# Performance work log

Hardware: AMD Instinct MI355X
Metric: run time of the kernel (lower is better)

Reference implementation:

```python
import jax, jax.numpy as jnp
import numpy as np

N = 20000   # mesh vertices
B = 8       # batch
F = 64      # in_channels
K = 6       # Chebyshev order
OUT = 64    # out_channels
NNZ = 320000  # nonzeros in sparse Laplacian (avg degree 16)


def setup_inputs() -> dict:
    key = jax.random.key(0)
    ks = jax.random.split(key, 6)
    x = jax.random.normal(ks[0], (B, N, F), dtype=jnp.float32)
    lap_rows = jax.random.randint(ks[1], (NNZ,), 0, N, dtype=jnp.int32)
    lap_cols = jax.random.randint(ks[2], (NNZ,), 0, N, dtype=jnp.int32)
    lap_vals = jax.random.normal(ks[3], (NNZ,), dtype=jnp.float32) * 0.05
    # fc: Linear(K*F, OUT), xavier_normal weight, zero bias
    W = jax.random.normal(ks[4], (OUT, K * F), dtype=jnp.float32) * float(np.sqrt(2.0 / (K * F + OUT)))
    b = jnp.zeros((OUT,), dtype=jnp.float32)
    return {"x": x, "lap_rows": lap_rows, "lap_cols": lap_cols,
            "lap_vals": lap_vals, "W": W, "b": b}


def reference(x, lap_rows, lap_cols, lap_vals, W, b):
    Bd, Nd, Fd = x.shape

    def spmm(v):  # sparse [N,N] @ dense [N, B*F] via COO gather + segment_sum
        return jax.ops.segment_sum(lap_vals[:, None] * v[lap_cols], lap_rows,
                                   num_segments=Nd)

    x0 = jnp.transpose(x, (1, 0, 2)).reshape(Nd, Bd * Fd)  # [N, B*F]
    outs = [x0]
    if K > 1:
        tx1 = spmm(x0)
        outs.append(tx1)
        tx0 = x0
        for _ in range(2, K):  # Chebyshev recurrence T_k = 2 L T_{k-1} - T_{k-2}
            tx2 = 2.0 * spmm(tx1) - tx0
            outs.append(tx2)
            tx0, tx1 = tx1, tx2
    out = jnp.concatenate([o.reshape(Nd, Bd, Fd) for o in outs], axis=2)  # [N,B,K*F]
    out = out.reshape(Nd * Bd, K * Fd) @ W.T + b  # dense fc
    return jnp.transpose(out.reshape(Nd, Bd, -1), (1, 0, 2))  # [B,N,OUT]
```

## Files before the change

kernel.cpp:

```cpp
#include <hip/hip_runtime.h>

#define N_V  20000
#define B_   8
#define F_   64
#define K_   6
#define OUT_ 64
#define NNZ_ 320000
#define BF   512
#define NSLICE 8
#define SLICE_W 2500
#define NBUK (N_V * NSLICE)
#define SCANB 157

typedef unsigned short ushort_t;
typedef unsigned int   uint_t;

using frag_ab = __attribute__((ext_vector_type(8))) short;
using frag_cd = __attribute__((ext_vector_type(4))) float;

__device__ __forceinline__ ushort_t f2bf(float f) {
    uint_t u = __float_as_uint(f);
    u += 0x7FFFu + ((u >> 16) & 1u);
    return (ushort_t)(u >> 16);
}
__device__ __forceinline__ uint_t pack2(float lo, float hi) {
    return (uint_t)f2bf(lo) | ((uint_t)f2bf(hi) << 16);
}
__device__ __forceinline__ void unpack2(uint_t u, float& lo, float& hi) {
    lo = __uint_as_float(u << 16);
    hi = __uint_as_float(u & 0xFFFF0000u);
}


__global__ void hist_kernel(const int* __restrict__ rows, const int* __restrict__ cols,
                            int* __restrict__ counts) {
    int e = blockIdx.x * 256 + threadIdx.x;
    if (e < NNZ_) {
        int key = (cols[e] / SLICE_W) * N_V + rows[e];
        atomicAdd(&counts[key], 1);
    }
}

__global__ __launch_bounds__(1024) void scan1(const int* __restrict__ counts,
                                              int* __restrict__ incl, int* __restrict__ bsum) {
    __shared__ int buf[1024];
    int tid = threadIdx.x;
    int i = blockIdx.x * 1024 + tid;
    int c = (i < NBUK) ? counts[i] : 0;
    buf[tid] = c;
    __syncthreads();
    for (int off = 1; off < 1024; off <<= 1) {
        int t = buf[tid];
        int add = (tid >= off) ? buf[tid - off] : 0;
        __syncthreads();
        buf[tid] = t + add;
        __syncthreads();
    }
    if (i < NBUK) incl[i] = buf[tid];
    if (tid == 1023) bsum[blockIdx.x] = buf[1023];
}

__global__ __launch_bounds__(256) void scan2(int* __restrict__ bsum) {
    __shared__ int buf[256];
    int tid = threadIdx.x;
    int c = (tid < SCANB) ? bsum[tid] : 0;
    buf[tid] = c;
    __syncthreads();
    for (int off = 1; off < 256; off <<= 1) {
        int t = buf[tid];
        int add = (tid >= off) ? buf[tid - off] : 0;
        __syncthreads();
        buf[tid] = t + add;
        __syncthreads();
    }
    if (tid < SCANB) bsum[tid] = buf[tid] - c;
}

__global__ __launch_bounds__(1024) void scan3(const int* __restrict__ counts,
                                              const int* __restrict__ bsum,
                                              int* __restrict__ bp, int* __restrict__ cursor) {
    int tid = threadIdx.x;
    int i = blockIdx.x * 1024 + tid;
    if (i < NBUK) {
        int p = bsum[blockIdx.x] + cursor[i];
        bp[i + 1] = p;
        cursor[i] = p - counts[i];
    }
    if (i == 0) bp[0] = 0;
}

__global__ void scatter_kernel(const int* __restrict__ rows, const int* __restrict__ cols,
                               const float* __restrict__ vals, int* __restrict__ cursor,
                               int2* __restrict__ edges) {
    int e = blockIdx.x * 256 + threadIdx.x;
    if (e < NNZ_) {
        int c = cols[e];
        int key = (c / SLICE_W) * N_V + rows[e];
        int pos = atomicAdd(&cursor[key], 1);
        int2 pe;
        pe.x = c;
        pe.y = __float_as_int(vals[e]);
        edges[pos] = pe;
    }
}

__global__ void prep_kernel(const float* __restrict__ x, uint_t* __restrict__ X0,
                            const float* __restrict__ W, ushort_t* __restrict__ Wfrag) {
    int blk = blockIdx.x;
    if (blk < 20000) {
        int idx = blk * 256 + threadIdx.x;
        int f2 = idx & 31;
        int b  = (idx >> 5) & 7;
        int n  = idx >> 8;
        float2 v = *(const float2*)&x[((size_t)b * N_V + n) * F_ + f2 * 2];
        X0[n * 256 + b * 32 + f2] = pack2(v.x, v.y);
    } else {
        int idx = (blk - 20000) * 256 + threadIdx.x;
        if (idx < 12 * 4 * 64 * 8) {
            int j    = idx & 7;
            int lane = (idx >> 3) & 63;
            int ct   = (idx >> 9) & 3;
            int s    = idx >> 11;
            int o     = ct * 16 + (lane & 15);
            int kglob = s * 32 + ((lane >> 4) & 3) * 8 + j;
            Wfrag[idx] = f2bf(W[o * (K_ * F_) + kglob]);
        }
    }
}

template <bool RECUR>
__global__ __launch_bounds__(256) void cheb_phase(const int* __restrict__ bp,
                                                  const int2* __restrict__ edges,
                                                  const ushort_t* __restrict__ Tprev,
                                                  const ushort_t* __restrict__ Tpp,
                                                  ushort_t* __restrict__ Tout) {
    const int wave = threadIdx.x >> 6, lane = threadIdx.x & 63;
    const int n0 = blockIdx.x * 8 + wave * 2;
    const int fo = lane * 8;

    float a0[8], a1[8];
#pragma unroll
    for (int i = 0; i < 8; ++i) { a0[i] = 0.f; a1[i] = 0.f; }

    for (int s = 0; s < NSLICE; ++s) {
        const int base = s * N_V + n0;
        const int st  = bp[base];
        const int mid = bp[base + 1];
        const int en  = bp[base + 2];
        for (int j = st; j < en; j += 4) {
            const int j1 = j + 1, j2 = j + 2, j3 = j + 3;
            const int c1 = min(j1, en - 1), c2 = min(j2, en - 1), c3 = min(j3, en - 1);
            int2 E0 = edges[j];
            int2 E1 = edges[c1];
            int2 E2 = edges[c2];
            int2 E3 = edges[c3];
            float v0 = __int_as_float(E0.y);
            float v1 = (j1 < en) ? __int_as_float(E1.y) : 0.f;
            float v2 = (j2 < en) ? __int_as_float(E2.y) : 0.f;
            float v3 = (j3 < en) ? __int_as_float(E3.y) : 0.f;
            uint4 u0 = *(const uint4*)(Tprev + (size_t)E0.x * BF + fo);
            uint4 u1 = *(const uint4*)(Tprev + (size_t)E1.x * BF + fo);
            uint4 u2 = *(const uint4*)(Tprev + (size_t)E2.x * BF + fo);
            uint4 u3 = *(const uint4*)(Tprev + (size_t)E3.x * BF + fo);
            float p00 = (j  < mid) ? v0 : 0.f, p01 = (j  < mid) ? 0.f : v0;
            float p10 = (j1 < mid) ? v1 : 0.f, p11 = (j1 < mid) ? 0.f : v1;
            float p20 = (j2 < mid) ? v2 : 0.f, p21 = (j2 < mid) ? 0.f : v2;
            float p30 = (j3 < mid) ? v3 : 0.f, p31 = (j3 < mid) ? 0.f : v3;
            float e0[8], e1[8], e2[8], e3[8];
            unpack2(u0.x, e0[0], e0[1]); unpack2(u0.y, e0[2], e0[3]);
            unpack2(u0.z, e0[4], e0[5]); unpack2(u0.w, e0[6], e0[7]);
            unpack2(u1.x, e1[0], e1[1]); unpack2(u1.y, e1[2], e1[3]);
            unpack2(u1.z, e1[4], e1[5]); unpack2(u1.w, e1[6], e1[7]);
            unpack2(u2.x, e2[0], e2[1]); unpack2(u2.y, e2[2], e2[3]);
            unpack2(u2.z, e2[4], e2[5]); unpack2(u2.w, e2[6], e2[7]);
            unpack2(u3.x, e3[0], e3[1]); unpack2(u3.y, e3[2], e3[3]);
            unpack2(u3.z, e3[4], e3[5]); unpack2(u3.w, e3[6], e3[7]);
#pragma unroll
            for (int i = 0; i < 8; ++i) {
                a0[i] = fmaf(p00, e0[i], a0[i]);
                a1[i] = fmaf(p01, e0[i], a1[i]);
                a0[i] = fmaf(p10, e1[i], a0[i]);
                a1[i] = fmaf(p11, e1[i], a1[i]);
                a0[i] = fmaf(p20, e2[i], a0[i]);
                a1[i] = fmaf(p21, e2[i], a1[i]);
                a0[i] = fmaf(p30, e3[i], a0[i]);
                a1[i] = fmaf(p31, e3[i], a1[i]);
            }
        }
    }

    {
        float res[8];
#pragma unroll
        for (int i = 0; i < 8; ++i) res[i] = a0[i];
        if (RECUR) {
            uint4 up = *(const uint4*)(Tpp + (size_t)n0 * BF + fo);
            float ep[8];
            unpack2(up.x, ep[0], ep[1]); unpack2(up.y, ep[2], ep[3]);
            unpack2(up.z, ep[4], ep[5]); unpack2(up.w, ep[6], ep[7]);
#pragma unroll
            for (int i = 0; i < 8; ++i) res[i] = 2.f * res[i] - ep[i];
        }
        uint4 st4;
        st4.x = pack2(res[0], res[1]);
        st4.y = pack2(res[2], res[3]);
        st4.z = pack2(res[4], res[5]);
        st4.w = pack2(res[6], res[7]);
        *(uint4*)(Tout + (size_t)n0 * BF + fo) = st4;
    }
    {
        float res[8];
#pragma unroll
        for (int i = 0; i < 8; ++i) res[i] = a1[i];
        if (RECUR) {
            uint4 up = *(const uint4*)(Tpp + (size_t)(n0 + 1) * BF + fo);
            float ep[8];
            unpack2(up.x, ep[0], ep[1]); unpack2(up.y, ep[2], ep[3]);
            unpack2(up.z, ep[4], ep[5]); unpack2(up.w, ep[6], ep[7]);
#pragma unroll
            for (int i = 0; i < 8; ++i) res[i] = 2.f * res[i] - ep[i];
        }
        uint4 st4;
        st4.x = pack2(res[0], res[1]);
        st4.y = pack2(res[2], res[3]);
        st4.z = pack2(res[4], res[5]);
        st4.w = pack2(res[6], res[7]);
        *(uint4*)(Tout + (size_t)(n0 + 1) * BF + fo) = st4;
    }
}

__global__ __launch_bounds__(256) void fc_mfma(const ushort_t* __restrict__ X0,
                                               const ushort_t* __restrict__ T1,
                                               const ushort_t* __restrict__ T2,
                                               const ushort_t* __restrict__ T3,
                                               const ushort_t* __restrict__ T4,
                                               const ushort_t* __restrict__ T5,
                                               const ushort_t* __restrict__ Wfrag,
                                               const float* __restrict__ bias,
                                               float* __restrict__ out) {
    const int wave = threadIdx.x >> 6, lane = threadIdx.x & 63;
    const int quad = lane >> 4, col = lane & 15;
    const int tb = blockIdx.x * 128 + wave * 32;
    const int r0 = tb + col, r1 = tb + 16 + col;
    const ushort_t* Tbuf[6] = {X0, T1, T2, T3, T4, T5};

    frag_cd acc0[4], acc1[4];
#pragma unroll
    for (int ct = 0; ct < 4; ++ct) {
        acc0[ct] = (frag_cd){0.f, 0.f, 0.f, 0.f};
        acc1[ct] = (frag_cd){0.f, 0.f, 0.f, 0.f};
    }

#pragma unroll
    for (int s = 0; s < 12; ++s) {
        const int f0 = (s & 1) * 32 + quad * 8;
        frag_ab fa0 = *(const frag_ab*)(Tbuf[s >> 1] + (size_t)r0 * F_ + f0);
        frag_ab fa1 = *(const frag_ab*)(Tbuf[s >> 1] + (size_t)r1 * F_ + f0);
#pragma unroll
        for (int ct = 0; ct < 4; ++ct) {
            frag_ab bfr = *(const frag_ab*)(Wfrag + (((s * 4 + ct) * 64 + lane) << 3));
            acc0[ct] = __builtin_amdgcn_mfma_f32_16x16x32_bf16(fa0, bfr, acc0[ct], 0, 0, 0);
            acc1[ct] = __builtin_amdgcn_mfma_f32_16x16x32_bf16(fa1, bfr, acc1[ct], 0, 0, 0);
        }
    }

#pragma unroll
    for (int ct = 0; ct < 4; ++ct) {
        const int o = ct * 16 + col;
        const float bv = bias[o];
#pragma unroll
        for (int reg = 0; reg < 4; ++reg) {
            int ra = tb + quad * 4 + reg;
            int rb = ra + 16;
            out[(size_t)(ra & 7) * N_V * OUT_ + (size_t)(ra >> 3) * OUT_ + o] = acc0[ct][reg] + bv;
            out[(size_t)(rb & 7) * N_V * OUT_ + (size_t)(rb >> 3) * OUT_ + o] = acc1[ct][reg] + bv;
        }
    }
}


extern "C" void kernel_launch(void* const* d_in, const int* in_sizes, int n_in,
                              void* d_out, int out_size, void* d_ws, size_t ws_size,
                              hipStream_t stream) {
    const float* x    = (const float*)d_in[0];
    const int*   rows = (const int*)  d_in[1];
    const int*   cols = (const int*)  d_in[2];
    const float* vals = (const float*)d_in[3];
    const float* W    = (const float*)d_in[4];
    const float* bias = (const float*)d_in[5];
    float* out = (float*)d_out;

    const size_t TSZ = (size_t)N_V * BF;
    ushort_t* T1 = (ushort_t*)d_ws;
    ushort_t* T2 = T1 + TSZ;
    ushort_t* T3 = T2 + TSZ;
    ushort_t* T4 = T3 + TSZ;
    ushort_t* T5 = T4 + TSZ;
    ushort_t* X0 = T5 + TSZ;
    ushort_t* Wfrag = X0 + TSZ;
    int* counts    = (int*)(Wfrag + 24576);
    int* bp        = counts + NBUK;
    int* cursor    = bp + NBUK + 64;
    int* bsum      = cursor + NBUK;
    int2* edges    = (int2*)(bsum + 256);

    hipMemsetAsync(counts, 0, NBUK * sizeof(int), stream);
    hist_kernel<<<(NNZ_ + 255) / 256, 256, 0, stream>>>(rows, cols, counts);
    scan1<<<SCANB, 1024, 0, stream>>>(counts, cursor, bsum);
    scan2<<<1, 256, 0, stream>>>(bsum);
    scan3<<<SCANB, 1024, 0, stream>>>(counts, bsum, bp, cursor);
    scatter_kernel<<<(NNZ_ + 255) / 256, 256, 0, stream>>>(rows, cols, vals, cursor, edges);
    prep_kernel<<<20096, 256, 0, stream>>>(x, (uint_t*)X0, W, Wfrag);

    cheb_phase<false><<<N_V / 8, 256, 0, stream>>>(bp, edges, X0, nullptr, T1);
    cheb_phase<true ><<<N_V / 8, 256, 0, stream>>>(bp, edges, T1, X0, T2);
    cheb_phase<true ><<<N_V / 8, 256, 0, stream>>>(bp, edges, T2, T1, T3);
    cheb_phase<true ><<<N_V / 8, 256, 0, stream>>>(bp, edges, T3, T2, T4);
    cheb_phase<true ><<<N_V / 8, 256, 0, stream>>>(bp, edges, T4, T3, T5);

    fc_mfma<<<(N_V * B_) / 128, 256, 0, stream>>>(X0, T1, T2, T3, T4, T5, Wfrag, bias, out);
}
```

Baseline: 393.0 us.

## Bucket edges by row pair with slice-minor keys and unroll gather by eight

Edge buckets are re-keyed as (row pair, column slice) instead of (slice, row), so each wave's edges for its two rows sit in one contiguous range. The row-parity bit is packed into the column index (bit 15), which removes the per-slice loop and the mid split. The gather loop now issues eight edge and feature loads per iteration to expose more memory parallelism. This shrinks the bucket and scan arrays but adds register pressure and relies on column indices fitting in 15 bits.

```diff
diff --git a/kernel.cpp b/kernel.cpp
--- a/kernel.cpp
+++ b/kernel.cpp
@@ -9,8 +9,9 @@
 #define BF   512
 #define NSLICE 8
 #define SLICE_W 2500
-#define NBUK (N_V * NSLICE)
-#define SCANB 157
+#define NPAIR (N_V / 2)
+#define NBUK (NPAIR * NSLICE)
+#define SCANB 79
 
 typedef unsigned short ushort_t;
 typedef unsigned int   uint_t;
@@ -36,7 +37,7 @@
                             int* __restrict__ counts) {
     int e = blockIdx.x * 256 + threadIdx.x;
     if (e < NNZ_) {
-        int key = (cols[e] / SLICE_W) * N_V + rows[e];
+        int key = (rows[e] >> 1) * NSLICE + cols[e] / SLICE_W;
         atomicAdd(&counts[key], 1);
     }
 }
@@ -95,10 +96,11 @@
     int e = blockIdx.x * 256 + threadIdx.x;
     if (e < NNZ_) {
         int c = cols[e];
-        int key = (c / SLICE_W) * N_V + rows[e];
+        int r = rows[e];
+        int key = (r >> 1) * NSLICE + c / SLICE_W;
         int pos = atomicAdd(&cursor[key], 1);
         int2 pe;
-        pe.x = c;
+        pe.x = c | ((r & 1) << 15);
         pe.y = __float_as_int(vals[e]);
         edges[pos] = pe;
     }
@@ -129,62 +131,45 @@
 }
 
 template <bool RECUR>
-__global__ __launch_bounds__(256) void cheb_phase(const int* __restrict__ bp,
-                                                  const int2* __restrict__ edges,
-                                                  const ushort_t* __restrict__ Tprev,
-                                                  const ushort_t* __restrict__ Tpp,
-                                                  ushort_t* __restrict__ Tout) {
+__global__ __launch_bounds__(256) void cheb_pair(const int* __restrict__ bp,
+                                                 const int2* __restrict__ edges,
+                                                 const ushort_t* __restrict__ Tprev,
+                                                 const ushort_t* __restrict__ Tpp,
+                                                 ushort_t* __restrict__ Tout) {
     const int wave = threadIdx.x >> 6, lane = threadIdx.x & 63;
-    const int n0 = blockIdx.x * 8 + wave * 2;
+    const int pair = blockIdx.x * 4 + wave;
+    const int n0 = pair * 2;
     const int fo = lane * 8;
+    const int st = bp[pair * NSLICE];
+    const int en = bp[pair * NSLICE + NSLICE];
 
     float a0[8], a1[8];
 #pragma unroll
     for (int i = 0; i < 8; ++i) { a0[i] = 0.f; a1[i] = 0.f; }
 
-    for (int s = 0; s < NSLICE; ++s) {
-        const int base = s * N_V + n0;
-        const int st  = bp[base];
-        const int mid = bp[base + 1];
-        const int en  = bp[base + 2];
-        for (int j = st; j < en; j += 4) {
-            const int j1 = j + 1, j2 = j + 2, j3 = j + 3;
-            const int c1 = min(j1, en - 1), c2 = min(j2, en - 1), c3 = min(j3, en - 1);
-            int2 E0 = edges[j];
-            int2 E1 = edges[c1];
-            int2 E2 = edges[c2];
-            int2 E3 = edges[c3];
-            float v0 = __int_as_float(E0.y);
-            float v1 = (j1 < en) ? __int_as_float(E1.y) : 0.f;
-            float v2 = (j2 < en) ? __int_as_float(E2.y) : 0.f;
-            float v3 = (j3 < en) ? __int_as_float(E3.y) : 0.f;
-            uint4 u0 = *(const uint4*)(Tprev + (size_t)E0.x * BF + fo);
-            uint4 u1 = *(const uint4*)(Tprev + (size_t)E1.x * BF + fo);
-            uint4 u2 = *(const uint4*)(Tprev + (size_t)E2.x * BF + fo);
-            uint4 u3 = *(const uint4*)(Tprev + (size_t)E3.x * BF + fo);
-            float p00 = (j  < mid) ? v0 : 0.f, p01 = (j  < mid) ? 0.f : v0;
-            float p10 = (j1 < mid) ? v1 : 0.f, p11 = (j1 < mid) ? 0.f : v1;
-            float p20 = (j2 < mid) ? v2 : 0.f, p21 = (j2 < mid) ? 0.f : v2;
-            float p30 = (j3 < mid) ? v3 : 0.f, p31 = (j3 < mid) ? 0.f : v3;
-            float e0[8], e1[8], e2[8], e3[8];
-            unpack2(u0.x, e0[0], e0[1]); unpack2(u0.y, e0[2], e0[3]);
-            unpack2(u0.z, e0[4], e0[5]); unpack2(u0.w, e0[6], e0[7]);
-            unpack2(u1.x, e1[0], e1[1]); unpack2(u1.y, e1[2], e1[3]);
-            unpack2(u1.z, e1[4], e1[5]); unpack2(u1.w, e1[6], e1[7]);
-            unpack2(u2.x, e2[0], e2[1]); unpack2(u2.y, e2[2], e2[3]);
-            unpack2(u2.z, e2[4], e2[5]); unpack2(u2.w, e2[6], e2[7]);
-            unpack2(u3.x, e3[0], e3[1]); unpack2(u3.y, e3[2], e3[3]);
-            unpack2(u3.z, e3[4], e3[5]); unpack2(u3.w, e3[6], e3[7]);
+    for (int j = st; j < en; j += 8) {
+        int2 E[8];
+#pragma unroll
+        for (int q = 0; q < 8; ++q) {
+            E[q] = edges[min(j + q, en - 1)];
+        }
+        uint4 u[8];
+#pragma unroll
+        for (int q = 0; q < 8; ++q) {
+            u[q] = *(const uint4*)(Tprev + (size_t)(E[q].x & 0x7FFF) * BF + fo);
+        }
+#pragma unroll
+        for (int q = 0; q < 8; ++q) {
+            const float v  = (j + q < en) ? __int_as_float(E[q].y) : 0.f;
+            const float p0 = (E[q].x & 0x8000) ? 0.f : v;
+            const float p1 = (E[q].x & 0x8000) ? v : 0.f;
+            float e[8];
+            unpack2(u[q].x, e[0], e[1]); unpack2(u[q].y, e[2], e[3]);
+            unpack2(u[q].z, e[4], e[5]); unpack2(u[q].w, e[6], e[7]);
 #pragma unroll
             for (int i = 0; i < 8; ++i) {
-                a0[i] = fmaf(p00, e0[i], a0[i]);
-                a1[i] = fmaf(p01, e0[i], a1[i]);
-                a0[i] = fmaf(p10, e1[i], a0[i]);
-                a1[i] = fmaf(p11, e1[i], a1[i]);
-                a0[i] = fmaf(p20, e2[i], a0[i]);
-                a1[i] = fmaf(p21, e2[i], a1[i]);
-                a0[i] = fmaf(p30, e3[i], a0[i]);
-                a1[i] = fmaf(p31, e3[i], a1[i]);
+                a0[i] = fmaf(p0, e[i], a0[i]);
+                a1[i] = fmaf(p1, e[i], a1[i]);
             }
         }
     }
@@ -312,11 +297,11 @@
     scatter_kernel<<<(NNZ_ + 255) / 256, 256, 0, stream>>>(rows, cols, vals, cursor, edges);
     prep_kernel<<<20096, 256, 0, stream>>>(x, (uint_t*)X0, W, Wfrag);
 
-    cheb_phase<false><<<N_V / 8, 256, 0, stream>>>(bp, edges, X0, nullptr, T1);
-    cheb_phase<true ><<<N_V / 8, 256, 0, stream>>>(bp, edges, T1, X0, T2);
-    cheb_phase<true ><<<N_V / 8, 256, 0, stream>>>(bp, edges, T2, T1, T3);
-    cheb_phase<true ><<<N_V / 8, 256, 0, stream>>>(bp, edges, T3, T2, T4);
-    cheb_phase<true ><<<N_V / 8, 256, 0, stream>>>(bp, edges, T4, T3, T5);
+    cheb_pair<false><<<NPAIR / 4, 256, 0, stream>>>(bp, edges, X0, nullptr, T1);
+    cheb_pair<true ><<<NPAIR / 4, 256, 0, stream>>>(bp, edges, T1, X0, T2);
+    cheb_pair<true ><<<NPAIR / 4, 256, 0, stream>>>(bp, edges, T2, T1, T3);
+    cheb_pair<true ><<<NPAIR / 4, 256, 0, stream>>>(bp, edges, T3, T2, T4);
+    cheb_pair<true ><<<NPAIR / 4, 256, 0, stream>>>(bp, edges, T4, T3, T5);
 
     fc_mfma<<<(N_V * B_) / 128, 256, 0, stream>>>(X0, T1, T2, T3, T4, T5, Wfrag, bias, out);
 }
```

Result: no change. 388.7 us (-1.1%).
